# Kernel tuning notes

Hardware: AMD Instinct MI355X
Metric: run time of the kernel (lower is better)

The kernel has to match this reference:

```python
import jax, jax.numpy as jnp
import numpy as np

RES = 32  # voxel grid resolution per axis (cfg.MODEL.NEURAL_POINTS.VOXEL_RES)


def upsample_ac(x, s):
    """Bilinear upsample with align_corners=True. x: [B,C,h,w] -> [B,C,h*s,w*s]."""
    if s == 1:
        return x
    B, C, h, w = x.shape
    H, W = h * s, w * s
    ys = jnp.arange(H, dtype=x.dtype) * ((h - 1) / (H - 1))
    xs = jnp.arange(W, dtype=x.dtype) * ((w - 1) / (W - 1))
    y0 = jnp.floor(ys).astype(jnp.int32)
    x0 = jnp.floor(xs).astype(jnp.int32)
    y1 = jnp.minimum(y0 + 1, h - 1)
    x1 = jnp.minimum(x0 + 1, w - 1)
    wy = (ys - y0.astype(x.dtype))[:, None]  # [H,1]
    wx = (xs - x0.astype(x.dtype))[None, :]  # [1,W]
    top = x[:, :, y0, :]
    bot = x[:, :, y1, :]
    a = top[..., x0]; b = top[..., x1]; c = bot[..., x0]; d = bot[..., x1]
    return (a * (1 - wx) + b * wx) * (1 - wy) + (c * (1 - wx) + d * wx) * wy


def vox_closest(pos):
    """construct_vox_points_closest: per occupied voxel, index of point closest to
    the voxel's point centroid. pos: [N,3] -> [RES^3] int32 indices."""
    N = pos.shape[0]
    Vn = RES ** 3
    mn = pos.min(0)
    mx = pos.max(0)
    vsz = (mx - mn) / RES  # obtain_voxel_size_based_grid_res
    coord = jnp.clip(jnp.floor((pos - mn) / vsz).astype(jnp.int32), 0, RES - 1)
    vid = (coord[:, 0] * RES + coord[:, 1]) * RES + coord[:, 2]  # [N]
    cnt = jax.ops.segment_sum(jnp.ones((N,), pos.dtype), vid, Vn)
    cen = jax.ops.segment_sum(pos, vid, Vn) / jnp.maximum(cnt, 1.0)[:, None]
    d = jnp.sum((pos - cen[vid]) ** 2, axis=-1)  # [N] dist^2 to own-voxel centroid
    dmin = jax.ops.segment_min(d, vid, Vn)
    cand = jnp.where(d <= dmin[vid], jnp.arange(N, dtype=jnp.int32), N)
    midx = jax.ops.segment_min(cand, vid, Vn)
    return jnp.where(midx >= N, 0, midx)  # guard (rare) empty voxels


def reference(rgb, f1, f2, f3, points_pos, points_dir, W1, b1, W2, b2, points_mask):
    V, _, H, W = rgb.shape
    N = V * H * W
    C = 59
    # valid_index = where(points_mask == 1) (mask is all ones -> identity gather)
    valid = jnp.nonzero(points_mask[0] == 1, size=N, fill_value=0)[0]
    pos = points_pos[0, valid]          # [N,3]
    pdir = points_dir[0, valid]         # [N,3]
    # project_point_feats: upsample each pyramid level to full res, concat channels
    ups = [upsample_ac(rgb, 1), upsample_ac(f1, 2), upsample_ac(f2, 4), upsample_ac(f3, 8)]
    pif = jnp.concatenate(ups, axis=1)                       # [V,59,H,W]
    pif = jnp.transpose(pif, (0, 2, 3, 1)).reshape(N, C)     # [N,59]
    color = jax.lax.stop_gradient(jnp.transpose(rgb, (0, 2, 3, 1)).reshape(N, 3))
    pif = pif[valid]
    color = color[valid]
    emb = jnp.concatenate([pif, pdir], axis=-1)              # [N,62]
    midx = vox_closest(pos)                                  # [32768]
    sel_emb = emb[midx]
    sel_pos = pos[midx]
    sel_color = color[midx]
    sel_dir = pdir[midx]
    # point_mlp (premlp_init): 62 -> 256 -> 256
    h = jax.nn.relu(sel_emb @ W1 + b1)
    points_embedding = h @ W2 + b2
    return points_embedding, sel_pos, sel_color, sel_dir


def setup_inputs() -> dict:
    key = jax.random.key(0)
    ks = jax.random.split(key, 10)
    V, H, W = 8, 240, 320
    N = V * H * W
    return {
        "rgb": jax.random.uniform(ks[0], (V, 3, H, W), jnp.float32),
        "f1": jax.random.normal(ks[1], (V, 8, H // 2, W // 2), jnp.float32),
        "f2": jax.random.normal(ks[2], (V, 16, H // 4, W // 4), jnp.float32),
        "f3": jax.random.normal(ks[3], (V, 32, H // 8, W // 8), jnp.float32),
        "points_pos": jax.random.uniform(ks[4], (1, N, 3), jnp.float32),
        "points_dir": jax.random.normal(ks[5], (1, N, 3), jnp.float32),
        "W1": jax.random.normal(ks[6], (62, 256), jnp.float32) * 0.05,
        "b1": jnp.zeros((256,), jnp.float32),
        "W2": jax.random.normal(ks[7], (256, 256), jnp.float32) * 0.05,
        "b2": jnp.zeros((256,), jnp.float32),
        "points_mask": jnp.ones((1, N), jnp.int32),
    }
```

## Files before the change

### kernel.cpp

```cpp
#include <hip/hip_runtime.h>
#include <hip/hip_bf16.h>
#include <limits.h>
#include <stddef.h>

#define NPTS   614400
#define RESV   32
#define NVOX   (RESV*RESV*RESV)
#define IMG_H  240
#define IMG_W  320
#define IMG_HW (IMG_H*IMG_W)
#define INF    __builtin_inff()
#define CAP    64
#define CAPP   32
#define SPILLCAP 4096

typedef __attribute__((ext_vector_type(8))) short short8;
typedef __attribute__((ext_vector_type(4))) short s16x4;
typedef __attribute__((ext_vector_type(4))) float f32x4;
typedef float f32x4u __attribute__((ext_vector_type(4), aligned(4)));

__device__ __forceinline__ float fadd_(float a, float b){
#pragma clang fp contract(off)
  return a + b;
}
__device__ __forceinline__ float fsub_(float a, float b){
#pragma clang fp contract(off)
  return a - b;
}
__device__ __forceinline__ float fmul_(float a, float b){
#pragma clang fp contract(off)
  return a * b;
}
__device__ __forceinline__ float fdiv_(float a, float b){
#pragma clang fp contract(off)
  return a / b;
}

__device__ __forceinline__ short f2bf(float x){
  __hip_bfloat16 h = __float2bfloat16(x);
  return *reinterpret_cast<short*>(&h);
}

__global__ void k_prep(int* __restrict__ cnt, int* __restrict__ spillcnt,
                       const float* __restrict__ W1, const float* __restrict__ W2,
                       short* __restrict__ W1t, short* __restrict__ W2t,
                       const float* __restrict__ pos,
                       f32x4* __restrict__ pmin, f32x4* __restrict__ pmax,
                       const float* __restrict__ f1, const float* __restrict__ f2,
                       const float* __restrict__ f3,
                       float* __restrict__ f1t, float* __restrict__ f2t,
                       float* __restrict__ f3t, int tposed){
  int gid = blockIdx.x*blockDim.x + threadIdx.x;
  int stride = gridDim.x*blockDim.x;
  if (gid < NVOX) cnt[gid] = 0;
  if (gid == 0) *spillcnt = 0;
  if (gid < 256*64){
    int n = gid >> 6, k = gid & 63;
    W1t[gid] = (k < 62) ? f2bf(W1[k*256 + n]) : (short)0;
  } else if (gid < 256*64 + 256*256){
    int j = gid - 256*64;
    int n = j >> 8, k = j & 255;
    W2t[j] = f2bf(W2[k*256 + n]);
  }

  if (tposed){
    for (int p = gid; p < 8*19200; p += stride){
      int img = p / 19200, pix = p - img*19200;
      const float* s = f1 + (size_t)img*8*19200 + pix;
      float r[8];
      #pragma unroll
      for (int c = 0; c < 8; c++) r[c] = s[(size_t)c*19200];
      float* d = f1t + (size_t)p*8;
      *(f32x4*)&d[0] = (f32x4){r[0],r[1],r[2],r[3]};
      *(f32x4*)&d[4] = (f32x4){r[4],r[5],r[6],r[7]};
    }
    for (int p = gid; p < 8*4800; p += stride){
      int img = p / 4800, pix = p - img*4800;
      const float* s = f2 + (size_t)img*16*4800 + pix;
      float* d = f2t + (size_t)p*16;
      #pragma unroll
      for (int cq = 0; cq < 4; cq++){
        f32x4 v = { s[(size_t)(4*cq+0)*4800], s[(size_t)(4*cq+1)*4800],
                    s[(size_t)(4*cq+2)*4800], s[(size_t)(4*cq+3)*4800] };
        *(f32x4*)&d[4*cq] = v;
      }
    }
    for (int p = gid; p < 8*1200; p += stride){
      int img = p / 1200, pix = p - img*1200;
      const float* s = f3 + (size_t)img*32*1200 + pix;
      float* d = f3t + (size_t)p*32;
      #pragma unroll
      for (int cq = 0; cq < 8; cq++){
        f32x4 v = { s[(size_t)(4*cq+0)*1200], s[(size_t)(4*cq+1)*1200],
                    s[(size_t)(4*cq+2)*1200], s[(size_t)(4*cq+3)*1200] };
        *(f32x4*)&d[4*cq] = v;
      }
    }
  }

  const f32x4* p4 = (const f32x4*)pos;
  float mn[3] = {  INF,  INF,  INF };
  float mx[3] = { -INF, -INF, -INF };
  for (int t = gid; t < NPTS/4; t += stride){
    f32x4 a = p4[3*t+0], b = p4[3*t+1], c = p4[3*t+2];
    mn[0] = fminf(mn[0], fminf(fminf(a.x, a.w), fminf(b.z, c.y)));
    mx[0] = fmaxf(mx[0], fmaxf(fmaxf(a.x, a.w), fmaxf(b.z, c.y)));
    mn[1] = fminf(mn[1], fminf(fminf(a.y, b.x), fminf(b.w, c.z)));
    mx[1] = fmaxf(mx[1], fmaxf(fmaxf(a.y, b.x), fmaxf(b.w, c.z)));
    mn[2] = fminf(mn[2], fminf(fminf(a.z, b.y), fminf(c.x, c.w)));
    mx[2] = fmaxf(mx[2], fmaxf(fmaxf(a.z, b.y), fmaxf(c.x, c.w)));
  }
  #pragma unroll
  for (int off = 32; off >= 1; off >>= 1){
    #pragma unroll
    for (int c = 0; c < 3; c++){
      mn[c] = fminf(mn[c], __shfl_down(mn[c], off, 64));
      mx[c] = fmaxf(mx[c], __shfl_down(mx[c], off, 64));
    }
  }
  __shared__ float smn[4][3], smx[4][3];
  int lane = threadIdx.x & 63, w = threadIdx.x >> 6;
  if (lane == 0){
    #pragma unroll
    for (int c = 0; c < 3; c++){ smn[w][c] = mn[c]; smx[w][c] = mx[c]; }
  }
  __syncthreads();
  if (threadIdx.x == 0){
    f32x4 a, b;
    a.x = fminf(fminf(smn[0][0], smn[1][0]), fminf(smn[2][0], smn[3][0]));
    a.y = fminf(fminf(smn[0][1], smn[1][1]), fminf(smn[2][1], smn[3][1]));
    a.z = fminf(fminf(smn[0][2], smn[1][2]), fminf(smn[2][2], smn[3][2]));
    a.w = 0.f;
    b.x = fmaxf(fmaxf(smx[0][0], smx[1][0]), fmaxf(smx[2][0], smx[3][0]));
    b.y = fmaxf(fmaxf(smx[0][1], smx[1][1]), fmaxf(smx[2][1], smx[3][1]));
    b.z = fmaxf(fmaxf(smx[0][2], smx[1][2]), fmaxf(smx[2][2], smx[3][2]));
    b.w = 0.f;
    pmin[blockIdx.x] = a;
    pmax[blockIdx.x] = b;
  }
}

__device__ __forceinline__ void reduce_minmax(const f32x4* __restrict__ pmin,
                                              const f32x4* __restrict__ pmax,
                                              float mn[3], float vsz[3]){
  int t = threadIdx.x;
  f32x4 a = pmin[t], b = pmin[t+256];
  f32x4 c = pmax[t], d = pmax[t+256];
  float lmn[3] = { fminf(a.x,b.x), fminf(a.y,b.y), fminf(a.z,b.z) };
  float lmx[3] = { fmaxf(c.x,d.x), fmaxf(c.y,d.y), fmaxf(c.z,d.z) };
  #pragma unroll
  for (int off = 32; off >= 1; off >>= 1){
    #pragma unroll
    for (int k = 0; k < 3; k++){
      lmn[k] = fminf(lmn[k], __shfl_xor(lmn[k], off, 64));
      lmx[k] = fmaxf(lmx[k], __shfl_xor(lmx[k], off, 64));
    }
  }
  __shared__ float smn[4][3], smx[4][3];
  int lane = t & 63, w = t >> 6;
  if (lane == 0){
    #pragma unroll
    for (int k = 0; k < 3; k++){ smn[w][k] = lmn[k]; smx[w][k] = lmx[k]; }
  }
  __syncthreads();
  #pragma unroll
  for (int k = 0; k < 3; k++){
    mn[k] = fminf(fminf(smn[0][k], smn[1][k]), fminf(smn[2][k], smn[3][k]));
    float mx = fmaxf(fmaxf(smx[0][k], smx[1][k]), fmaxf(smx[2][k], smx[3][k]));
    vsz[k] = fdiv_(fsub_(mx, mn[k]), 32.0f);
  }
}

__global__ void k_scatter(const float* __restrict__ pos,
                          const f32x4* __restrict__ pmin, const f32x4* __restrict__ pmax,
                          int* __restrict__ cnt, int* __restrict__ slots,
                          int* __restrict__ spillcnt, int2* __restrict__ spill,
                          f32x4* __restrict__ slotpos, int haspp){
  float mn[3], vsz[3];
  reduce_minmax(pmin, pmax, mn, vsz);

  int t = blockIdx.x*blockDim.x + threadIdx.x;
  const f32x4* p4 = (const f32x4*)pos;
  f32x4 a = p4[3*t+0], b = p4[3*t+1], c = p4[3*t+2];
  float X[4] = {a.x, a.w, b.z, c.y};
  float Y[4] = {a.y, b.x, b.w, c.z};
  float Z[4] = {a.z, b.y, c.x, c.w};
  #pragma unroll
  for (int j = 0; j < 4; j++){
    int i = 4*t + j;
    float P[3] = {X[j], Y[j], Z[j]};
    int v = 0;
    #pragma unroll
    for (int k = 0; k < 3; k++){
      float tt = fdiv_(fsub_(P[k], mn[k]), vsz[k]);
      int cc = (int)floorf(tt);
      cc = min(max(cc, 0), RESV-1);
      v = v*RESV + cc;
    }
    int p = atomicAdd(&cnt[v], 1);
    if (haspp && p < CAPP){
      f32x4 e = { P[0], P[1], P[2], __int_as_float(i) };
      slotpos[(size_t)v*CAPP + p] = e;
    }
    if (p < CAP){
      slots[v*CAP + p] = i;
    } else {
      int sp = atomicAdd(spillcnt, 1);
      if (sp < SPILLCAP){ int2 e; e.x = v; e.y = i; spill[sp] = e; }
    }
  }
}

__launch_bounds__(256)
__global__ void k_voxfull(const int* __restrict__ cnt, const int* __restrict__ slots,
                          const int* __restrict__ spillcnt, const int2* __restrict__ spill,
                          const f32x4* __restrict__ slotpos, int haspp,
                          const float* __restrict__ pos,
                          const float* __restrict__ pdir, const float* __restrict__ rgb,
                          const float* __restrict__ f1, const float* __restrict__ f2,
                          const float* __restrict__ f3,
                          const float* __restrict__ f1t, const float* __restrict__ f2t,
                          const float* __restrict__ f3t, int tposed,
                          float* __restrict__ selpos, float* __restrict__ selcol,
                          float* __restrict__ seldir, short* __restrict__ emb){
  __shared__ __align__(16) int skey[4][64];
  __shared__ f32x4 sposl[4][64];
  int lane = threadIdx.x & 63;
  int wv   = threadIdx.x >> 6;
  int v = blockIdx.x*4 + wv;

  f32x4 q = {0.f, 0.f, 0.f, 0.f};
  if (haspp) q = slotpos[(size_t)v*CAPP + (lane & (CAPP-1))];
  int n = cnt[v];

  int m = 0;
  unsigned long long ball = 0;
  float px = 0.f, py = 0.f, pz = 0.f;

  if (n > CAP){
    if (lane == 0){
      int sc = min(*spillcnt, SPILLCAP);
      float sx = 0.f, sy = 0.f, sz = 0.f; int last = -1;
      for (int i = 0; i < n; i++){
        int best = INT_MAX;
        for (int j = 0; j < CAP; j++){
          int id = slots[v*CAP + j];
          if (id > last && id < best) best = id;
        }
        for (int j = 0; j < sc; j++){
          int2 e = spill[j];
          if (e.x == v && e.y > last && e.y < best) best = e.y;
        }
        sx = fadd_(sx, pos[3*best+0]);
        sy = fadd_(sy, pos[3*best+1]);
        sz = fadd_(sz, pos[3*best+2]);
        last = best;
      }
      float cf = (float)n;
      float cx = fdiv_(sx, cf), cy = fdiv_(sy, cf), cz = fdiv_(sz, cf);
      float dmin = INF; int mm = 0;
      for (int j = 0; j < CAP + sc; j++){
        int id; int ok = 1;
        if (j < CAP) id = slots[v*CAP + j];
        else { int2 e = spill[j-CAP]; ok = (e.x == v); id = e.y; }
        if (!ok) continue;
        float dx = fsub_(pos[3*id+0], cx);
        float dy = fsub_(pos[3*id+1], cy);
        float dz = fsub_(pos[3*id+2], cz);
        float d  = fadd_(fadd_(fmul_(dx,dx), fmul_(dy,dy)), fmul_(dz,dz));
        if (d < dmin || (d == dmin && id < mm)){ dmin = d; mm = id; }
      }
      m = mm;
    }
    m = __shfl(m, 0, 64);
  } else {
    int key = INT_MAX;
    if (haspp && n <= CAPP){
      if (lane < n){
        px = q.x; py = q.y; pz = q.z;
        key = __float_as_int(q.w);
      }
    } else {
      if (lane < n){
        key = slots[v*CAP + lane];
        if (key < NPTS-1){
          f32x4u qq = *(const f32x4u*)&pos[3*key];
          px = qq.x; py = qq.y; pz = qq.z;
        } else {
          px = pos[3*key+0]; py = pos[3*key+1]; pz = pos[3*key+2];
        }
      }
    }

    skey[wv][lane] = key;
    __builtin_amdgcn_wave_barrier();
    int r = 0;
    {
      int nq = (n + 3) >> 2;
      const int4* k4 = (const int4*)&skey[wv][0];
      for (int j = 0; j < nq; j++){
        int4 kk = k4[j];
        r += (kk.x < key) + (kk.y < key) + (kk.z < key) + (kk.w < key);
      }
    }
    if (lane < n){
      f32x4 e = { px, py, pz, 0.f };
      sposl[wv][r] = e;
    }
    __builtin_amdgcn_wave_barrier();

    float sx = 0.f, sy = 0.f, sz = 0.f;
    for (int i = 0; i < n; i++){
      f32x4 pp = sposl[wv][i];
      sx = fadd_(sx, pp.x);
      sy = fadd_(sy, pp.y);
      sz = fadd_(sz, pp.z);
    }
    float cf = fmaxf((float)n, 1.0f);
    float cx = fdiv_(sx, cf), cy = fdiv_(sy, cf), cz = fdiv_(sz, cf);

    float bd = INF; int bi = 0;
    if (lane < n){
      float dx = fsub_(px, cx), dy = fsub_(py, cy), dz = fsub_(pz, cz);
      bd = fadd_(fadd_(fmul_(dx,dx), fmul_(dy,dy)), fmul_(dz,dz));
      bi = key;
    }
    #pragma unroll
    for (int off = 32; off >= 1; off >>= 1){
      float od = __shfl_xor(bd, off, 64);
      int   oi = __shfl_xor(bi, off, 64);
      if (od < bd || (od == bd && oi < bi)){ bd = od; bi = oi; }
    }
    m = bi;
    ball = __ballot(lane < n && key == m);
  }

  float wx_ = 0.f, wy_ = 0.f, wz_ = 0.f;
  if (ball){
    int wl = (int)(__ffsll((long long)ball) - 1);
    wx_ = __shfl(px, wl, 64);
    wy_ = __shfl(py, wl, 64);
    wz_ = __shfl(pz, wl, 64);
  }

  int img = m / IMG_HW;
  int rem = m - img*IMG_HW;
  int y = rem / IMG_W;
  int x = rem - y*IMG_W;
  int ch = lane;
  float val;
  if (ch < 3){
    val = rgb[((img*3 + ch)*IMG_H + y)*IMG_W + x];
    selcol[3*v+ch] = val;
    float sp = ball ? ((ch == 0) ? wx_ : (ch == 1) ? wy_ : wz_) : pos[3*m+ch];
    selpos[3*v+ch] = sp;
  } else if (ch < 59){
    int lvl = (ch >= 27) ? 2 : ((ch >= 11) ? 1 : 0);
    int c   = ch - ((lvl == 0) ? 3 : ((lvl == 1) ? 11 : 27));
    int C   = 8 << lvl;
    int h   = 120 >> lvl, w = 160 >> lvl;
    float ry = (lvl == 0) ? (119.0f/239.0f) : ((lvl == 1) ? (59.0f/239.0f) : (29.0f/239.0f));
    float rx = (lvl == 0) ? (159.0f/319.0f) : ((lvl == 1) ? (79.0f/319.0f) : (39.0f/319.0f));
    float ys = (float)y * ry;
    float xs = (float)x * rx;
    int y0 = (int)floorf(ys);
    int x0 = (int)floorf(xs);
    int y1 = min(y0+1, h-1);
    int x1 = min(x0+1, w-1);
    float wy = ys - (float)y0;
    float wx = xs - (float)x0;
    float aa, bb, cc, dd;
    if (tposed){
      const float* ft = (lvl == 0) ? f1t : ((lvl == 1) ? f2t : f3t);
      const float* base = ft + (size_t)(img*h*w)*C + c;
      aa = base[(y0*w + x0)*C];
      bb = base[(y0*w + x1)*C];
      cc = base[(y1*w + x0)*C];
      dd = base[(y1*w + x1)*C];
    } else {
      const float* f = (lvl == 0) ? f1 : ((lvl == 1) ? f2 : f3);
      const float* plane = f + ((size_t)img*C + c)*(size_t)(h*w);
      aa = plane[y0*w + x0];
      bb = plane[y0*w + x1];
      cc = plane[y1*w + x0];
      dd = plane[y1*w + x1];
    }
    val = (aa*(1.f-wx) + bb*wx)*(1.f-wy) + (cc*(1.f-wx) + dd*wx)*wy;
  } else if (ch < 62){
    val = pdir[3*m + (ch-59)];
    seldir[3*v+(ch-59)] = val;
  } else {
    val = 0.f;
  }
  emb[(size_t)v*64 + ch] = f2bf(val);
}

#define MLP_BLOCKS 512
#define MLP_TILES  (NVOX/16/MLP_BLOCKS)
__launch_bounds__(256, 2)
__global__ void k_mlp(const short* __restrict__ emb, const short* __restrict__ W1t,
                      const float* __restrict__ b1f, const short* __restrict__ W2t,
                      const float* __restrict__ b2f, float* __restrict__ out){
  __shared__ short Hs[16][264];
  int t    = threadIdx.x;
  int lane = t & 63;
  int wv   = t >> 6;
  int m    = lane & 15;
  int q    = lane >> 4;

  short8 w1f[4][2], w2f[4][8];
  float  b1r[4][4], b2r[4];
  #pragma unroll
  for (int nt = 0; nt < 4; nt++){
    int n = wv*64 + nt*16 + m;
    #pragma unroll
    for (int kq = 0; kq < 2; kq++)
      w1f[nt][kq] = *(const short8*)&W1t[(size_t)n*64 + kq*32 + q*8];
    #pragma unroll
    for (int kq = 0; kq < 8; kq++)
      w2f[nt][kq] = *(const short8*)&W2t[(size_t)n*256 + kq*32 + q*8];
    #pragma unroll
    for (int i = 0; i < 4; i++)
      b1r[nt][i] = b1f[wv*64 + nt*16 + q*4 + i];
    b2r[nt] = b2f[n];
  }

  for (int tt = 0; tt < MLP_TILES; tt++){
    int row0 = (blockIdx.x*MLP_TILES + tt)*16;

    short8 ef0 = *(const short8*)&emb[(size_t)(row0 + m)*64 + q*8];
    short8 ef1 = *(const short8*)&emb[(size_t)(row0 + m)*64 + 32 + q*8];

    #pragma unroll
    for (int nt = 0; nt < 4; nt++){
      f32x4 c = {0.f, 0.f, 0.f, 0.f};
      c = __builtin_amdgcn_mfma_f32_16x16x32_bf16(w1f[nt][0], ef0, c, 0, 0, 0);
      c = __builtin_amdgcn_mfma_f32_16x16x32_bf16(w1f[nt][1], ef1, c, 0, 0, 0);
      s16x4 hv;
      #pragma unroll
      for (int i = 0; i < 4; i++)
        hv[i] = f2bf(fmaxf(c[i] + b1r[nt][i], 0.f));
      *(s16x4*)&Hs[m][wv*64 + nt*16 + q*4] = hv;
    }
    __syncthreads();

    f32x4 acc[4] = {{0,0,0,0},{0,0,0,0},{0,0,0,0},{0,0,0,0}};
    #pragma unroll
    for (int kq = 0; kq < 8; kq++){
      short8 af = *(const short8*)&Hs[m][kq*32 + q*8];
      #pragma unroll
      for (int nt = 0; nt < 4; nt++)
        acc[nt] = __builtin_amdgcn_mfma_f32_16x16x32_bf16(af, w2f[nt][kq], acc[nt], 0, 0, 0);
    }
    __syncthreads();

    #pragma unroll
    for (int nt = 0; nt < 4; nt++){
      int n = wv*64 + nt*16 + m;
      #pragma unroll
      for (int i = 0; i < 4; i++)
        out[(size_t)(row0 + q*4 + i)*256 + n] = acc[nt][i] + b2r[nt];
    }
  }
}

extern "C" void kernel_launch(void* const* d_in, const int* in_sizes, int n_in,
                              void* d_out, int out_size, void* d_ws, size_t ws_size,
                              hipStream_t stream){
  const float* rgb  = (const float*)d_in[0];
  const float* f1   = (const float*)d_in[1];
  const float* f2   = (const float*)d_in[2];
  const float* f3   = (const float*)d_in[3];
  const float* pos  = (const float*)d_in[4];
  const float* pdir = (const float*)d_in[5];
  const float* W1   = (const float*)d_in[6];
  const float* b1   = (const float*)d_in[7];
  const float* W2   = (const float*)d_in[8];
  const float* b2   = (const float*)d_in[9];

  float* out      = (float*)d_out;
  float* out_emb  = out;
  float* out_pos  = out + (size_t)NVOX*256;
  float* out_col  = out_pos + (size_t)NVOX*3;
  float* out_dir  = out_col + (size_t)NVOX*3;

  char* w = (char*)d_ws;
  int*   spillcnt = (int*)w;       w += 64;
  f32x4* pmin     = (f32x4*)w;     w += (size_t)512*16;
  f32x4* pmax     = (f32x4*)w;     w += (size_t)512*16;
  int*   cnt      = (int*)w;       w += (size_t)NVOX*4;
  short* W1t      = (short*)w;     w += (size_t)256*64*2;
  short* W2t      = (short*)w;     w += (size_t)256*256*2;
  short* emb      = (short*)w;     w += (size_t)NVOX*64*2;
  int2*  spill    = (int2*)w;      w += (size_t)SPILLCAP*8;
  int*   slots    = (int*)w;       w += (size_t)NVOX*CAP*4;
  float* f1t      = (float*)w;     w += (size_t)8*19200*8*4;
  float* f2t      = (float*)w;     w += (size_t)8*4800*16*4;
  float* f3t      = (float*)w;     w += (size_t)8*1200*32*4;
  int tposed = ((size_t)(w - (char*)d_ws) <= ws_size) ? 1 : 0;
  f32x4* slotpos  = (f32x4*)w;     w += (size_t)NVOX*CAPP*16;
  int haspp = ((size_t)(w - (char*)d_ws) <= ws_size) ? 1 : 0;

  k_prep    <<<512,    256, 0, stream>>>(cnt, spillcnt, W1, W2, W1t, W2t, pos, pmin, pmax,
                                         f1, f2, f3, f1t, f2t, f3t, tposed);
  k_scatter <<<NPTS/1024, 256, 0, stream>>>(pos, pmin, pmax, cnt, slots, spillcnt, spill,
                                            slotpos, haspp);
  k_voxfull <<<NVOX/4, 256, 0, stream>>>(cnt, slots, spillcnt, spill, slotpos, haspp,
                                         pos, pdir, rgb, f1, f2, f3,
                                         f1t, f2t, f3t, tposed,
                                         out_pos, out_col, out_dir, emb);
  k_mlp     <<<MLP_BLOCKS, 256, 0, stream>>>(emb, W1t, b1, W2t, b2, out_emb);
}
```

Baseline: 192.5 us.

## Scatter one point per thread and skip duplicate slot writes when slotpos exists

The scatter kernel now processes one point per thread with scalar position loads instead of four points per thread with vector loads, and the grid is widened to match. When the packed slotpos buffer is available, the first CAPP entries of a voxel are stored only in slotpos rather than in both slotpos and slots, which cuts write traffic. The voxel kernel reads ids from slotpos for those entries in both the overflow path and the n>CAPP path. This raises thread count and makes position loads less coalesced, in exchange for fewer redundant global stores and more atomic parallelism.

```diff
diff --git a/kernel.cpp b/kernel.cpp
--- a/kernel.cpp
+++ b/kernel.cpp
@@ -179,29 +179,28 @@
   float mn[3], vsz[3];
   reduce_minmax(pmin, pmax, mn, vsz);
 
-  int t = blockIdx.x*blockDim.x + threadIdx.x;
-  const f32x4* p4 = (const f32x4*)pos;
-  f32x4 a = p4[3*t+0], b = p4[3*t+1], c = p4[3*t+2];
-  float X[4] = {a.x, a.w, b.z, c.y};
-  float Y[4] = {a.y, b.x, b.w, c.z};
-  float Z[4] = {a.z, b.y, c.x, c.w};
+  int i = blockIdx.x*blockDim.x + threadIdx.x;
+  float P[3] = { pos[3*i+0], pos[3*i+1], pos[3*i+2] };
+  int v = 0;
   #pragma unroll
-  for (int j = 0; j < 4; j++){
-    int i = 4*t + j;
-    float P[3] = {X[j], Y[j], Z[j]};
-    int v = 0;
-    #pragma unroll
-    for (int k = 0; k < 3; k++){
-      float tt = fdiv_(fsub_(P[k], mn[k]), vsz[k]);
-      int cc = (int)floorf(tt);
-      cc = min(max(cc, 0), RESV-1);
-      v = v*RESV + cc;
-    }
-    int p = atomicAdd(&cnt[v], 1);
-    if (haspp && p < CAPP){
+  for (int k = 0; k < 3; k++){
+    float tt = fdiv_(fsub_(P[k], mn[k]), vsz[k]);
+    int cc = (int)floorf(tt);
+    cc = min(max(cc, 0), RESV-1);
+    v = v*RESV + cc;
+  }
+  int p = atomicAdd(&cnt[v], 1);
+  if (haspp){
+    if (p < CAPP){
       f32x4 e = { P[0], P[1], P[2], __int_as_float(i) };
       slotpos[(size_t)v*CAPP + p] = e;
-    }
+    } else if (p < CAP){
+      slots[v*CAP + p] = i;
+    } else {
+      int sp = atomicAdd(spillcnt, 1);
+      if (sp < SPILLCAP){ int2 e; e.x = v; e.y = i; spill[sp] = e; }
+    }
+  } else {
     if (p < CAP){
       slots[v*CAP + p] = i;
     } else {
@@ -244,7 +243,8 @@
       for (int i = 0; i < n; i++){
         int best = INT_MAX;
         for (int j = 0; j < CAP; j++){
-          int id = slots[v*CAP + j];
+          int id = (haspp && j < CAPP) ? __float_as_int(slotpos[(size_t)v*CAPP + j].w)
+                                       : slots[v*CAP + j];
           if (id > last && id < best) best = id;
         }
         for (int j = 0; j < sc; j++){
@@ -261,8 +261,10 @@
       float dmin = INF; int mm = 0;
       for (int j = 0; j < CAP + sc; j++){
         int id; int ok = 1;
-        if (j < CAP) id = slots[v*CAP + j];
-        else { int2 e = spill[j-CAP]; ok = (e.x == v); id = e.y; }
+        if (j < CAP){
+          id = (haspp && j < CAPP) ? __float_as_int(slotpos[(size_t)v*CAPP + j].w)
+                                   : slots[v*CAP + j];
+        } else { int2 e = spill[j-CAP]; ok = (e.x == v); id = e.y; }
         if (!ok) continue;
         float dx = fsub_(pos[3*id+0], cx);
         float dy = fsub_(pos[3*id+1], cy);
@@ -279,6 +281,19 @@
       if (lane < n){
         px = q.x; py = q.y; pz = q.z;
         key = __float_as_int(q.w);
+      }
+    } else if (haspp){
+      if (lane < CAPP){
+        px = q.x; py = q.y; pz = q.z;
+        key = __float_as_int(q.w);
+      } else if (lane < n){
+        key = slots[v*CAP + lane];
+        if (key < NPTS-1){
+          f32x4u qq = *(const f32x4u*)&pos[3*key];
+          px = qq.x; py = qq.y; pz = qq.z;
+        } else {
+          px = pos[3*key+0]; py = pos[3*key+1]; pz = pos[3*key+2];
+        }
       }
     } else {
       if (lane < n){
@@ -503,8 +518,8 @@
 
   k_prep    <<<512,    256, 0, stream>>>(cnt, spillcnt, W1, W2, W1t, W2t, pos, pmin, pmax,
                                          f1, f2, f3, f1t, f2t, f3t, tposed);
-  k_scatter <<<NPTS/1024, 256, 0, stream>>>(pos, pmin, pmax, cnt, slots, spillcnt, spill,
-                                            slotpos, haspp);
+  k_scatter <<<NPTS/256, 256, 0, stream>>>(pos, pmin, pmax, cnt, slots, spillcnt, spill,
+                                           slotpos, haspp);
   k_voxfull <<<NVOX/4, 256, 0, stream>>>(cnt, slots, spillcnt, spill, slotpos, haspp,
                                          pos, pdir, rgb, f1, f2, f3,
                                          f1t, f2t, f3t, tposed,
```

Result: no change. 195.7 us (+1.7%).
